# Kernel tuning notes

Measured on AMD Instinct MI355X. Metric: run time of the kernel, lower is better.

Reference implementation:

```python
import jax, jax.numpy as jnp
import numpy as np

LAMBDA = 0.01

def setup_inputs() -> dict:
    key = jax.random.key(0)
    x = jax.random.normal(key, (32, 16384, 64), dtype=jnp.float32)
    return {"x": x}

def reference(x):
    # x: (B, N, D)
    B, N, D = x.shape
    mean = jnp.mean(x, axis=1, keepdims=True)          # (B, 1, D)
    diffs = x - mean                                    # (B, N, D)
    # Fused covariance: sum of centered outer products == GEMM, no (B,N,D,D) blowup
    cov = jnp.einsum('bnd,bne->bde', diffs, diffs) / (N - 1)  # (B, D, D)
    cov = cov + LAMBDA * jnp.eye(D, dtype=x.dtype)
    # torch.unique on the flattened symmetric matrices == globally sorted set of the
    # B * D*(D+1)/2 distinct entries (duplicates only arise from symmetry, prob-1 for
    # continuous inputs). Extract upper triangle per batch, then global sort.
    iu, ju = jnp.triu_indices(D)
    tri = cov[:, iu, ju]                                # (B, d_out)
    d_out = D * (D + 1) // 2
    return jnp.sort(tri.reshape(-1)).reshape(B, d_out)
```

## Files before the change

### kernel.cpp

```cpp
#include <hip/hip_runtime.h>
#include <hip/hip_bf16.h>
#include <stdint.h>


#define BATCHES 32
#define NSAMP   16384
#define DIM     64
#define LAMBDA  0.01f
#define NTRI    2080
#define NOUT    (BATCHES * NTRI)

#define CHUNKS_PER_BATCH 32
#define SAMP_PER_BLOCK   (NSAMP / CHUNKS_PER_BATCH)
#define SAMP_PER_WAVE    (SAMP_PER_BLOCK / 4)
#define PARTIAL_STRIDE   2624

#define KEY_SHIFT 14
#define NBUCKET   (1 << 18)
#define SMALL_MAX 64u
#define SORT_CAP  8192

typedef __attribute__((ext_vector_type(4))) float f32x4;
typedef __attribute__((ext_vector_type(8))) short s16x8;

__device__ __forceinline__ uint32_t sort_key(float v) {
    uint32_t u = __builtin_bit_cast(uint32_t, v);
    return u ^ (uint32_t)(((int32_t)u >> 31) | 0x80000000u);
}

__device__ __forceinline__ uint32_t cvt_pk_bf16(float lo, float hi) {
    __hip_bfloat162 bb = __float22bfloat162_rn(make_float2(lo, hi));
    uint32_t u;
    __builtin_memcpy(&u, &bb, 4);
    return u;
}

__constant__ const int c_tmi[10] = {0, 0, 0, 0, 1, 1, 1, 2, 2, 3};
__constant__ const int c_tni[10] = {0, 1, 2, 3, 1, 2, 3, 2, 3, 3};

struct CovLds {
    float red[2][64][41];
    float msum_red[4][64];
};

template <typename EpilogueFn>
__device__ __forceinline__ void cov_body(const float* __restrict__ x, CovLds& L,
                                         EpilogueFn epi) {
    const int tid  = threadIdx.x;
    const int wave = tid >> 6;
    const int lane = tid & 63;
    const int b     = blockIdx.x / CHUNKS_PER_BATCH;
    const int chunk = blockIdx.x % CHUNKS_PER_BATCH;
    const int n_start = chunk * SAMP_PER_BLOCK + wave * SAMP_PER_WAVE;

    const int l15  = lane & 15;
    const int quad = lane >> 4;

    const float* xw = x + ((size_t)b * NSAMP + n_start) * DIM
                        + quad * 8 * DIM + l15;

    f32x4 acc[10];
#pragma unroll
    for (int t = 0; t < 10; ++t) acc[t] = (f32x4){0.f, 0.f, 0.f, 0.f};
    float sum_t[4] = {0.f, 0.f, 0.f, 0.f};

    float va[8][4], vb[8][4];

    auto loadit = [&](float (&v)[8][4], int kc) {
        const float* xs = xw + kc * 32 * DIM;
#pragma unroll
        for (int j = 0; j < 8; ++j)
#pragma unroll
            for (int t = 0; t < 4; ++t)
                v[j][t] = xs[j * DIM + t * 16];
    };

    auto compute = [&](float (&v)[8][4]) {
#pragma unroll
        for (int j = 0; j < 8; ++j)
#pragma unroll
            for (int t = 0; t < 4; ++t) sum_t[t] += v[j][t];

        s16x8 frag[4];
#pragma unroll
        for (int t = 0; t < 4; ++t) {
            uint32_t pk0 = cvt_pk_bf16(v[0][t], v[1][t]);
            uint32_t pk1 = cvt_pk_bf16(v[2][t], v[3][t]);
            uint32_t pk2 = cvt_pk_bf16(v[4][t], v[5][t]);
            uint32_t pk3 = cvt_pk_bf16(v[6][t], v[7][t]);
            frag[t] = __builtin_bit_cast(s16x8, make_uint4(pk0, pk1, pk2, pk3));
        }

        acc[0] = __builtin_amdgcn_mfma_f32_16x16x32_bf16(frag[0], frag[0], acc[0], 0, 0, 0);
        acc[1] = __builtin_amdgcn_mfma_f32_16x16x32_bf16(frag[0], frag[1], acc[1], 0, 0, 0);
        acc[2] = __builtin_amdgcn_mfma_f32_16x16x32_bf16(frag[0], frag[2], acc[2], 0, 0, 0);
        acc[3] = __builtin_amdgcn_mfma_f32_16x16x32_bf16(frag[0], frag[3], acc[3], 0, 0, 0);
        acc[4] = __builtin_amdgcn_mfma_f32_16x16x32_bf16(frag[1], frag[1], acc[4], 0, 0, 0);
        acc[5] = __builtin_amdgcn_mfma_f32_16x16x32_bf16(frag[1], frag[2], acc[5], 0, 0, 0);
        acc[6] = __builtin_amdgcn_mfma_f32_16x16x32_bf16(frag[1], frag[3], acc[6], 0, 0, 0);
        acc[7] = __builtin_amdgcn_mfma_f32_16x16x32_bf16(frag[2], frag[2], acc[7], 0, 0, 0);
        acc[8] = __builtin_amdgcn_mfma_f32_16x16x32_bf16(frag[2], frag[3], acc[8], 0, 0, 0);
        acc[9] = __builtin_amdgcn_mfma_f32_16x16x32_bf16(frag[3], frag[3], acc[9], 0, 0, 0);
    };

    loadit(va, 0);
    loadit(vb, 1);
    compute(va);
    loadit(va, 2);
    compute(vb);
    loadit(vb, 3);
    compute(va);
    compute(vb);

#pragma unroll
    for (int t = 0; t < 4; ++t) {
        sum_t[t] += __shfl_xor(sum_t[t], 16, 64);
        sum_t[t] += __shfl_xor(sum_t[t], 32, 64);
    }
    if (lane < 16) {
#pragma unroll
        for (int t = 0; t < 4; ++t) L.msum_red[wave][t * 16 + lane] = sum_t[t];
    }

    __syncthreads();
    if (wave == 1 || wave == 3) {
        int slot = wave >> 1;
#pragma unroll
        for (int t = 0; t < 10; ++t)
#pragma unroll
            for (int r = 0; r < 4; ++r) L.red[slot][lane][t * 4 + r] = acc[t][r];
    }
    __syncthreads();
    if (wave == 0 || wave == 2) {
        int slot = wave >> 1;
#pragma unroll
        for (int t = 0; t < 10; ++t)
#pragma unroll
            for (int r = 0; r < 4; ++r) acc[t][r] += L.red[slot][lane][t * 4 + r];
    }
    __syncthreads();
    if (wave == 2) {
#pragma unroll
        for (int t = 0; t < 10; ++t)
#pragma unroll
            for (int r = 0; r < 4; ++r) L.red[0][lane][t * 4 + r] = acc[t][r];
    }
    __syncthreads();
    if (wave == 0) {
#pragma unroll
        for (int t = 0; t < 10; ++t)
#pragma unroll
            for (int r = 0; r < 4; ++r) acc[t][r] += L.red[0][lane][t * 4 + r];
        float msum_tot = L.msum_red[0][lane] + L.msum_red[1][lane] +
                         L.msum_red[2][lane] + L.msum_red[3][lane];
        epi(b, lane, quad, l15, acc, msum_tot);
    }
}

__global__ __launch_bounds__(256, 3) void cov_kernel_p(const float* __restrict__ x,
                                                       float* __restrict__ partials,
                                                       uint32_t* __restrict__ hist,
                                                       uint32_t* __restrict__ counts) {
    hist[blockIdx.x * 256 + threadIdx.x] = 0u;
    if (blockIdx.x == 0 && threadIdx.x < 16) counts[threadIdx.x] = 0u;

    __shared__ CovLds L;
    float* Pb = partials + (size_t)blockIdx.x * PARTIAL_STRIDE;
    cov_body(x, L, [&](int b, int lane, int quad, int l15, f32x4* acc, float msum) {
#pragma unroll
        for (int t = 0; t < 10; ++t)
#pragma unroll
            for (int r = 0; r < 4; ++r)
                Pb[t * 256 + r * 64 + lane] = acc[t][r];
        Pb[2560 + lane] = msum;
    });
}

__global__ __launch_bounds__(256, 3) void cov_kernel_a(const float* __restrict__ x,
                                                       float* __restrict__ S,
                                                       float* __restrict__ Msum) {
    __shared__ CovLds L;
    cov_body(x, L, [&](int b, int lane, int quad, int l15, f32x4* acc, float msum) {
        float* Sb = S + b * DIM * DIM;
#pragma unroll
        for (int t = 0; t < 10; ++t) {
            int d0 = c_tmi[t] * 16 + quad * 4;
            int e  = c_tni[t] * 16 + l15;
#pragma unroll
            for (int r = 0; r < 4; ++r)
                atomicAdd(&Sb[(d0 + r) * DIM + e], acc[t][r]);
        }
        atomicAdd(&Msum[b * DIM + lane], msum);
    });
}

__global__ __launch_bounds__(256) void reduce_kernel(const float* __restrict__ partials,
                                                     float* __restrict__ tri,
                                                     uint32_t* __restrict__ hist) {
    const int b = blockIdx.x / 10, k = blockIdx.x % 10;
    const int tid = threadIdx.x;
    __shared__ float msum[DIM];
    const float* P0 = partials + (size_t)b * CHUNKS_PER_BATCH * PARTIAL_STRIDE;

    if (tid < DIM) {
        float ms = 0.f;
#pragma unroll
        for (int c = 0; c < CHUNKS_PER_BATCH; ++c)
            ms += P0[c * PARTIAL_STRIDE + 2560 + tid];
        msum[tid] = ms;
    }

    float a = 0.f;
#pragma unroll
    for (int c = 0; c < CHUNKS_PER_BATCH; ++c)
        a += P0[c * PARTIAL_STRIDE + k * 256 + tid];
    __syncthreads();

    const int r = tid >> 6, lane = tid & 63, quad = lane >> 4, l15 = lane & 15;
    const int row = c_tmi[k] * 16 + quad * 4 + r;
    const int col = c_tni[k] * 16 + l15;
    if (row <= col) {
        float v = (a - msum[row] * msum[col] * (1.0f / NSAMP)) * (1.0f / (NSAMP - 1));
        if (row == col) v += LAMBDA;
        int p = row * 64 - (row * (row + 1)) / 2 + col;
        tri[b * NTRI + p] = v;
        atomicAdd(&hist[sort_key(v) >> KEY_SHIFT], 1u);
    }
}

__global__ void finalize_kernel(const float* __restrict__ S,
                                const float* __restrict__ Msum,
                                float* __restrict__ tri,
                                uint32_t* __restrict__ hist) {
    int t = blockIdx.x * blockDim.x + threadIdx.x;
    int b = t >> 12, de = t & 4095, d = de >> 6, e = de & 63;
    if (d > e) return;
    float ssum = S[b * 4096 + d * 64 + e];
    float md = Msum[b * 64 + d], me = Msum[b * 64 + e];
    float v = (ssum - md * me * (1.0f / NSAMP)) * (1.0f / (NSAMP - 1));
    if (d == e) v += LAMBDA;
    int p = d * 64 - (d * (d + 1)) / 2 + e;
    tri[b * NTRI + p] = v;
    atomicAdd(&hist[sort_key(v) >> KEY_SHIFT], 1u);
}

__global__ __launch_bounds__(256) void scanA_kernel(const uint32_t* __restrict__ hist,
                                                    uint32_t* __restrict__ blocksums) {
    __shared__ uint32_t s[256];
    int tid = threadIdx.x;
    s[tid] = hist[blockIdx.x * 256 + tid];
    __syncthreads();
    for (int off = 128; off > 0; off >>= 1) {
        if (tid < off) s[tid] += s[tid + off];
        __syncthreads();
    }
    if (tid == 0) blocksums[blockIdx.x] = s[0];
}

__global__ __launch_bounds__(256) void scanB_kernel(const uint32_t* __restrict__ hist,
                                                    const uint32_t* __restrict__ blocksums,
                                                    uint32_t* __restrict__ offsets,
                                                    uint2* __restrict__ wl_small,
                                                    uint2* __restrict__ wl_large,
                                                    uint32_t* __restrict__ counts) {
    __shared__ uint32_t bs[256];
    __shared__ uint32_t sc[256];
    __shared__ uint32_t base_sh;
    int tid = threadIdx.x, bid = blockIdx.x;

    uint32_t b4[4]; uint32_t s4 = 0;
#pragma unroll
    for (int i = 0; i < 4; ++i) { b4[i] = blocksums[4 * tid + i]; s4 += b4[i]; }
    bs[tid] = s4;
    __syncthreads();
    for (int off = 1; off < 256; off <<= 1) {
        uint32_t a = (tid >= off) ? bs[tid - off] : 0u;
        __syncthreads();
        bs[tid] += a;
        __syncthreads();
    }
    if (tid == (bid >> 2)) {
        uint32_t base = (tid > 0) ? bs[tid - 1] : 0u;
        for (int i = 0; i < (bid & 3); ++i) base += b4[i];
        base_sh = base;
    }

    uint32_t v = hist[bid * 256 + tid];
    sc[tid] = v;
    __syncthreads();
    for (int off = 1; off < 256; off <<= 1) {
        uint32_t a = (tid >= off) ? sc[tid - off] : 0u;
        __syncthreads();
        sc[tid] += a;
        __syncthreads();
    }
    uint32_t excl = base_sh + sc[tid] - v;
    offsets[bid * 256 + tid] = excl;
    if (v >= 2u) {
        if (v <= SMALL_MAX) {
            uint32_t w = atomicAdd(&counts[0], 1u);
            wl_small[w] = make_uint2(excl, v);
        } else {
            uint32_t w = atomicAdd(&counts[1], 1u);
            wl_large[w] = make_uint2(excl, v);
        }
    }
}

__global__ void scatter_kernel(const float* __restrict__ tri,
                               uint32_t* __restrict__ offsets,
                               float* __restrict__ out) {
    int i = blockIdx.x * blockDim.x + threadIdx.x;
    if (i >= NOUT) return;
    float v = tri[i];
    uint32_t pos = atomicAdd(&offsets[sort_key(v) >> KEY_SHIFT], 1u);
    out[pos] = v;
}

__global__ __launch_bounds__(256) void runsort_kernel(float* __restrict__ out,
                                                      const uint2* __restrict__ wl_small,
                                                      const uint2* __restrict__ wl_large,
                                                      const uint32_t* __restrict__ counts) {
    __shared__ float buf[SORT_CAP];

    uint32_t nl = counts[1];
    for (uint32_t w = blockIdx.x; w < nl; w += gridDim.x) {
        uint2 ent = wl_large[w];
        uint32_t start = ent.x, cnt = ent.y;
        if (cnt > SORT_CAP) continue;
        uint32_t m = 1;
        while (m < cnt) m <<= 1;
        for (uint32_t i = threadIdx.x; i < m; i += blockDim.x)
            buf[i] = (i < cnt) ? out[start + i] : __builtin_inff();
        __syncthreads();
        for (uint32_t k = 2; k <= m; k <<= 1) {
            for (uint32_t j = k >> 1; j > 0; j >>= 1) {
                for (uint32_t i = threadIdx.x; i < m; i += blockDim.x) {
                    uint32_t ixj = i ^ j;
                    if (ixj > i) {
                        float a = buf[i], c = buf[ixj];
                        bool up = ((i & k) == 0u);
                        if ((a > c) == up) { buf[i] = c; buf[ixj] = a; }
                    }
                }
                __syncthreads();
            }
        }
        for (uint32_t i = threadIdx.x; i < cnt; i += blockDim.x)
            out[start + i] = buf[i];
        __syncthreads();
    }

    uint32_t ns = counts[0];
    int wave = threadIdx.x >> 6, lane = threadIdx.x & 63;
    for (uint32_t r = blockIdx.x * 4 + wave; r < ns; r += gridDim.x * 4) {
        uint2 e = wl_small[r];
        uint32_t start = e.x, cnt = e.y;
        float v = (lane < (int)cnt) ? out[start + lane] : __builtin_inff();
#pragma unroll
        for (uint32_t k = 2; k <= 64; k <<= 1)
            for (uint32_t j = k >> 1; j > 0; j >>= 1) {
                float p = __shfl_xor(v, (int)j, 64);
                bool keepmin = (((lane & k) == 0u) == ((lane & j) == 0u));
                v = keepmin ? fminf(v, p) : fmaxf(v, p);
            }
        if (lane < (int)cnt) out[start + lane] = v;
    }
}

static void launch_tail(uint32_t* hist, uint32_t* blocksums, uint32_t* offsets,
                        float* tri, uint2* wl_small, uint2* wl_large,
                        uint32_t* counts, float* out, hipStream_t stream) {
    scanA_kernel<<<NBUCKET / 256, 256, 0, stream>>>(hist, blocksums);
    scanB_kernel<<<NBUCKET / 256, 256, 0, stream>>>(hist, blocksums, offsets,
                                                    wl_small, wl_large, counts);
    scatter_kernel<<<(NOUT + 255) / 256, 256, 0, stream>>>(tri, offsets, out);
    runsort_kernel<<<1024, 256, 0, stream>>>(out, wl_small, wl_large, counts);
}

extern "C" void kernel_launch(void* const* d_in, const int* in_sizes, int n_in,
                              void* d_out, int out_size, void* d_ws, size_t ws_size,
                              hipStream_t stream) {
    const float* x = (const float*)d_in[0];
    float* out = (float*)d_out;
    char* ws = (char*)d_ws;

    const size_t NEED_P = 2666560 + (size_t)1024 * PARTIAL_STRIDE * 4;

    if (ws_size >= NEED_P) {
        uint32_t* hist      = (uint32_t*)(ws);
        uint32_t* counts    = (uint32_t*)(ws + 1048576);
        uint32_t* offsets   = (uint32_t*)(ws + 1048640);
        uint32_t* blocksums = (uint32_t*)(ws + 2097216);
        float*    tri       = (float*)(ws + 2101312);
        uint2*    wl_small  = (uint2*)(ws + 2367552);
        uint2*    wl_large  = (uint2*)(ws + 2633792);
        float*    partials  = (float*)(ws + 2666560);

        cov_kernel_p<<<BATCHES * CHUNKS_PER_BATCH, 256, 0, stream>>>(x, partials, hist, counts);
        reduce_kernel<<<BATCHES * 10, 256, 0, stream>>>(partials, tri, hist);
        launch_tail(hist, blocksums, offsets, tri, wl_small, wl_large, counts, out, stream);
    } else {
        float*    S         = (float*)(ws);
        float*    Msum      = (float*)(ws + 524288);
        uint32_t* hist      = (uint32_t*)(ws + 532480);
        uint32_t* counts    = (uint32_t*)(ws + 1581056);
        uint32_t* offsets   = (uint32_t*)(ws + 1581120);
        uint32_t* blocksums = (uint32_t*)(ws + 2629696);
        float*    tri       = (float*)(ws + 2633792);
        uint2*    wl_small  = (uint2*)(ws + 2900032);
        uint2*    wl_large  = (uint2*)(ws + 3166272);

        (void)hipMemsetAsync(d_ws, 0, 1581120, stream);
        cov_kernel_a<<<BATCHES * CHUNKS_PER_BATCH, 256, 0, stream>>>(x, S, Msum);
        finalize_kernel<<<(BATCHES * 4096) / 256, 256, 0, stream>>>(S, Msum, tri, hist);
        launch_tail(hist, blocksums, offsets, tri, wl_small, wl_large, counts, out, stream);
    }
}
```

Baseline: 302.2 us.

## Fuse reduce, scan, scatter and run-sort into one cooperative kernel with grid syncs

Replaces the five separate tail launches (reduce, scanA, scanB, scatter, runsort) with a single cooperative kernel of 512 persistent blocks that loops over work units and separates the phases with grid-wide syncs. The goal is to remove per-launch overhead and the idle gaps between the small dependent kernels. In exchange, each phase now runs on a fixed grid with grid.sync barriers and a union of LDS buffers, which can lower per-phase parallelism (e.g. scanA/scanB had 1024 blocks). It also depends on cooperative launch succeeding, and the launch's return value is ignored.

```diff
diff --git a/kernel.cpp b/kernel.cpp
--- a/kernel.cpp
+++ b/kernel.cpp
@@ -1,6 +1,9 @@
 #include <hip/hip_runtime.h>
 #include <hip/hip_bf16.h>
+#include <hip/hip_cooperative_groups.h>
 #include <stdint.h>
+
+namespace cg = cooperative_groups;
 
 
 #define BATCHES 32
@@ -19,6 +22,8 @@
 #define NBUCKET   (1 << 18)
 #define SMALL_MAX 64u
 #define SORT_CAP  8192
+
+#define TAIL_BLOCKS 512
 
 typedef __attribute__((ext_vector_type(4))) float f32x4;
 typedef __attribute__((ext_vector_type(8))) short s16x8;
@@ -194,12 +199,12 @@
     });
 }
 
-__global__ __launch_bounds__(256) void reduce_kernel(const float* __restrict__ partials,
-                                                     float* __restrict__ tri,
-                                                     uint32_t* __restrict__ hist) {
-    const int b = blockIdx.x / 10, k = blockIdx.x % 10;
-    const int tid = threadIdx.x;
-    __shared__ float msum[DIM];
+
+__device__ __forceinline__ void reduce_unit(const float* __restrict__ partials,
+                                            float* __restrict__ tri,
+                                            uint32_t* __restrict__ hist,
+                                            float* msum_sh, int unit, int tid) {
+    const int b = unit / 10, k = unit % 10;
     const float* P0 = partials + (size_t)b * CHUNKS_PER_BATCH * PARTIAL_STRIDE;
 
     if (tid < DIM) {
@@ -207,7 +212,7 @@
 #pragma unroll
         for (int c = 0; c < CHUNKS_PER_BATCH; ++c)
             ms += P0[c * PARTIAL_STRIDE + 2560 + tid];
-        msum[tid] = ms;
+        msum_sh[tid] = ms;
     }
 
     float a = 0.f;
@@ -220,54 +225,36 @@
     const int row = c_tmi[k] * 16 + quad * 4 + r;
     const int col = c_tni[k] * 16 + l15;
     if (row <= col) {
-        float v = (a - msum[row] * msum[col] * (1.0f / NSAMP)) * (1.0f / (NSAMP - 1));
+        float v = (a - msum_sh[row] * msum_sh[col] * (1.0f / NSAMP)) * (1.0f / (NSAMP - 1));
         if (row == col) v += LAMBDA;
         int p = row * 64 - (row * (row + 1)) / 2 + col;
         tri[b * NTRI + p] = v;
         atomicAdd(&hist[sort_key(v) >> KEY_SHIFT], 1u);
     }
-}
-
-__global__ void finalize_kernel(const float* __restrict__ S,
-                                const float* __restrict__ Msum,
-                                float* __restrict__ tri,
-                                uint32_t* __restrict__ hist) {
-    int t = blockIdx.x * blockDim.x + threadIdx.x;
-    int b = t >> 12, de = t & 4095, d = de >> 6, e = de & 63;
-    if (d > e) return;
-    float ssum = S[b * 4096 + d * 64 + e];
-    float md = Msum[b * 64 + d], me = Msum[b * 64 + e];
-    float v = (ssum - md * me * (1.0f / NSAMP)) * (1.0f / (NSAMP - 1));
-    if (d == e) v += LAMBDA;
-    int p = d * 64 - (d * (d + 1)) / 2 + e;
-    tri[b * NTRI + p] = v;
-    atomicAdd(&hist[sort_key(v) >> KEY_SHIFT], 1u);
-}
-
-__global__ __launch_bounds__(256) void scanA_kernel(const uint32_t* __restrict__ hist,
-                                                    uint32_t* __restrict__ blocksums) {
-    __shared__ uint32_t s[256];
-    int tid = threadIdx.x;
-    s[tid] = hist[blockIdx.x * 256 + tid];
+    __syncthreads();
+}
+
+__device__ __forceinline__ void scanA_unit(const uint32_t* __restrict__ hist,
+                                           uint32_t* __restrict__ blocksums,
+                                           uint32_t* s, int u, int tid) {
+    s[tid] = hist[u * 256 + tid];
     __syncthreads();
     for (int off = 128; off > 0; off >>= 1) {
         if (tid < off) s[tid] += s[tid + off];
         __syncthreads();
     }
-    if (tid == 0) blocksums[blockIdx.x] = s[0];
-}
-
-__global__ __launch_bounds__(256) void scanB_kernel(const uint32_t* __restrict__ hist,
-                                                    const uint32_t* __restrict__ blocksums,
-                                                    uint32_t* __restrict__ offsets,
-                                                    uint2* __restrict__ wl_small,
-                                                    uint2* __restrict__ wl_large,
-                                                    uint32_t* __restrict__ counts) {
-    __shared__ uint32_t bs[256];
-    __shared__ uint32_t sc[256];
-    __shared__ uint32_t base_sh;
-    int tid = threadIdx.x, bid = blockIdx.x;
-
+    if (tid == 0) blocksums[u] = s[0];
+    __syncthreads();
+}
+
+__device__ __forceinline__ void scanB_unit(const uint32_t* __restrict__ hist,
+                                           const uint32_t* __restrict__ blocksums,
+                                           uint32_t* __restrict__ offsets,
+                                           uint2* __restrict__ wl_small,
+                                           uint2* __restrict__ wl_large,
+                                           uint32_t* __restrict__ counts,
+                                           uint32_t* bs, uint32_t* sc,
+                                           uint32_t* base_sh, int u, int tid) {
     uint32_t b4[4]; uint32_t s4 = 0;
 #pragma unroll
     for (int i = 0; i < 4; ++i) { b4[i] = blocksums[4 * tid + i]; s4 += b4[i]; }
@@ -279,13 +266,13 @@
         bs[tid] += a;
         __syncthreads();
     }
-    if (tid == (bid >> 2)) {
+    if (tid == (u >> 2)) {
         uint32_t base = (tid > 0) ? bs[tid - 1] : 0u;
-        for (int i = 0; i < (bid & 3); ++i) base += b4[i];
-        base_sh = base;
-    }
-
-    uint32_t v = hist[bid * 256 + tid];
+        for (int i = 0; i < (u & 3); ++i) base += b4[i];
+        *base_sh = base;
+    }
+
+    uint32_t v = hist[u * 256 + tid];
     sc[tid] = v;
     __syncthreads();
     for (int off = 1; off < 256; off <<= 1) {
@@ -294,8 +281,8 @@
         sc[tid] += a;
         __syncthreads();
     }
-    uint32_t excl = base_sh + sc[tid] - v;
-    offsets[bid * 256 + tid] = excl;
+    uint32_t excl = *base_sh + sc[tid] - v;
+    offsets[u * 256 + tid] = excl;
     if (v >= 2u) {
         if (v <= SMALL_MAX) {
             uint32_t w = atomicAdd(&counts[0], 1u);
@@ -305,24 +292,14 @@
             wl_large[w] = make_uint2(excl, v);
         }
     }
-}
-
-__global__ void scatter_kernel(const float* __restrict__ tri,
-                               uint32_t* __restrict__ offsets,
-                               float* __restrict__ out) {
-    int i = blockIdx.x * blockDim.x + threadIdx.x;
-    if (i >= NOUT) return;
-    float v = tri[i];
-    uint32_t pos = atomicAdd(&offsets[sort_key(v) >> KEY_SHIFT], 1u);
-    out[pos] = v;
-}
-
-__global__ __launch_bounds__(256) void runsort_kernel(float* __restrict__ out,
-                                                      const uint2* __restrict__ wl_small,
-                                                      const uint2* __restrict__ wl_large,
-                                                      const uint32_t* __restrict__ counts) {
-    __shared__ float buf[SORT_CAP];
-
+    __syncthreads();
+}
+
+__device__ __forceinline__ void runsort_body(float* __restrict__ out,
+                                             const uint2* __restrict__ wl_small,
+                                             const uint2* __restrict__ wl_large,
+                                             const uint32_t* __restrict__ counts,
+                                             float* buf) {
     uint32_t nl = counts[1];
     for (uint32_t w = blockIdx.x; w < nl; w += gridDim.x) {
         uint2 ent = wl_large[w];
@@ -368,6 +345,99 @@
     }
 }
 
+union TailLds {
+    float    red_msum[DIM];
+    uint32_t scanA_s[256];
+    struct { uint32_t bs[256]; uint32_t sc[256]; uint32_t base; } sb;
+    float    buf[SORT_CAP];
+};
+
+__global__ __launch_bounds__(256, 2) void tail_kernel(
+        const float* __restrict__ partials, float* __restrict__ tri,
+        uint32_t* __restrict__ hist, uint32_t* __restrict__ blocksums,
+        uint32_t* __restrict__ offsets, uint2* __restrict__ wl_small,
+        uint2* __restrict__ wl_large, uint32_t* __restrict__ counts,
+        float* __restrict__ out) {
+    cg::grid_group grid = cg::this_grid();
+    __shared__ TailLds L;
+    const int tid = threadIdx.x;
+
+    for (int u = blockIdx.x; u < BATCHES * 10; u += gridDim.x)
+        reduce_unit(partials, tri, hist, L.red_msum, u, tid);
+    grid.sync();
+
+    for (int u = blockIdx.x; u < NBUCKET / 256; u += gridDim.x)
+        scanA_unit(hist, blocksums, L.scanA_s, u, tid);
+    grid.sync();
+
+    for (int u = blockIdx.x; u < NBUCKET / 256; u += gridDim.x)
+        scanB_unit(hist, blocksums, offsets, wl_small, wl_large, counts,
+                   L.sb.bs, L.sb.sc, &L.sb.base, u, tid);
+    grid.sync();
+
+    for (int i = blockIdx.x * 256 + tid; i < NOUT; i += gridDim.x * 256) {
+        float v = tri[i];
+        uint32_t pos = atomicAdd(&offsets[sort_key(v) >> KEY_SHIFT], 1u);
+        out[pos] = v;
+    }
+    grid.sync();
+
+    runsort_body(out, wl_small, wl_large, counts, L.buf);
+}
+
+__global__ void finalize_kernel(const float* __restrict__ S,
+                                const float* __restrict__ Msum,
+                                float* __restrict__ tri,
+                                uint32_t* __restrict__ hist) {
+    int t = blockIdx.x * blockDim.x + threadIdx.x;
+    int b = t >> 12, de = t & 4095, d = de >> 6, e = de & 63;
+    if (d > e) return;
+    float ssum = S[b * 4096 + d * 64 + e];
+    float md = Msum[b * 64 + d], me = Msum[b * 64 + e];
+    float v = (ssum - md * me * (1.0f / NSAMP)) * (1.0f / (NSAMP - 1));
+    if (d == e) v += LAMBDA;
+    int p = d * 64 - (d * (d + 1)) / 2 + e;
+    tri[b * NTRI + p] = v;
+    atomicAdd(&hist[sort_key(v) >> KEY_SHIFT], 1u);
+}
+
+__global__ __launch_bounds__(256) void scanA_kernel(const uint32_t* __restrict__ hist,
+                                                    uint32_t* __restrict__ blocksums) {
+    __shared__ uint32_t s[256];
+    scanA_unit(hist, blocksums, s, blockIdx.x, threadIdx.x);
+}
+
+__global__ __launch_bounds__(256) void scanB_kernel(const uint32_t* __restrict__ hist,
+                                                    const uint32_t* __restrict__ blocksums,
+                                                    uint32_t* __restrict__ offsets,
+                                                    uint2* __restrict__ wl_small,
+                                                    uint2* __restrict__ wl_large,
+                                                    uint32_t* __restrict__ counts) {
+    __shared__ uint32_t bs[256];
+    __shared__ uint32_t sc[256];
+    __shared__ uint32_t base_sh;
+    scanB_unit(hist, blocksums, offsets, wl_small, wl_large, counts,
+               bs, sc, &base_sh, blockIdx.x, threadIdx.x);
+}
+
+__global__ void scatter_kernel(const float* __restrict__ tri,
+                               uint32_t* __restrict__ offsets,
+                               float* __restrict__ out) {
+    int i = blockIdx.x * blockDim.x + threadIdx.x;
+    if (i >= NOUT) return;
+    float v = tri[i];
+    uint32_t pos = atomicAdd(&offsets[sort_key(v) >> KEY_SHIFT], 1u);
+    out[pos] = v;
+}
+
+__global__ __launch_bounds__(256) void runsort_kernel(float* __restrict__ out,
+                                                      const uint2* __restrict__ wl_small,
+                                                      const uint2* __restrict__ wl_large,
+                                                      const uint32_t* __restrict__ counts) {
+    __shared__ float buf[SORT_CAP];
+    runsort_body(out, wl_small, wl_large, counts, buf);
+}
+
 static void launch_tail(uint32_t* hist, uint32_t* blocksums, uint32_t* offsets,
                         float* tri, uint2* wl_small, uint2* wl_large,
                         uint32_t* counts, float* out, hipStream_t stream) {
@@ -398,8 +468,11 @@
         float*    partials  = (float*)(ws + 2666560);
 
         cov_kernel_p<<<BATCHES * CHUNKS_PER_BATCH, 256, 0, stream>>>(x, partials, hist, counts);
-        reduce_kernel<<<BATCHES * 10, 256, 0, stream>>>(partials, tri, hist);
-        launch_tail(hist, blocksums, offsets, tri, wl_small, wl_large, counts, out, stream);
+
+        void* args[9] = {&partials, &tri, &hist, &blocksums, &offsets,
+                         &wl_small, &wl_large, &counts, &out};
+        (void)hipLaunchCooperativeKernel(reinterpret_cast<void*>(tail_kernel),
+                                         dim3(TAIL_BLOCKS), dim3(256), args, 0, stream);
     } else {
         float*    S         = (float*)(ws);
         float*    Msum      = (float*)(ws + 524288);
```

New measurement: 464.3 us. +53.6%, slower.

## Replace two-pass histogram scan with single-pass decoupled look-back scan

Applied to the files above, without the earlier changes.

Merges the scanA/scanB pair into one scan kernel that uses decoupled look-back. Each block publishes its aggregate or inclusive prefix through a flag-tagged word in scan_state, and one wave per block spins over its predecessors. The scan_state words are zeroed in the covariance kernel. This removes one kernel launch and the blocksums round trip. The cost is spin-waiting, which depends on blocks being scheduled roughly in index order.

```diff
diff --git a/kernel.cpp b/kernel.cpp
--- a/kernel.cpp
+++ b/kernel.cpp
@@ -17,6 +17,7 @@
 
 #define KEY_SHIFT 14
 #define NBUCKET   (1 << 18)
+#define SCAN_BLOCKS (NBUCKET / 256)
 #define SMALL_MAX 64u
 #define SORT_CAP  8192
 
@@ -160,8 +161,10 @@
 __global__ __launch_bounds__(256, 3) void cov_kernel_p(const float* __restrict__ x,
                                                        float* __restrict__ partials,
                                                        uint32_t* __restrict__ hist,
-                                                       uint32_t* __restrict__ counts) {
+                                                       uint32_t* __restrict__ counts,
+                                                       uint32_t* __restrict__ scan_state) {
     hist[blockIdx.x * 256 + threadIdx.x] = 0u;
+    if (threadIdx.x == 0) scan_state[blockIdx.x] = 0u;
     if (blockIdx.x == 0 && threadIdx.x < 16) counts[threadIdx.x] = 0u;
 
     __shared__ CovLds L;
@@ -244,6 +247,92 @@
     atomicAdd(&hist[sort_key(v) >> KEY_SHIFT], 1u);
 }
 
+__global__ __launch_bounds__(256) void scan_kernel(const uint32_t* __restrict__ hist,
+                                                   uint32_t* __restrict__ offsets,
+                                                   uint32_t* __restrict__ scan_state,
+                                                   uint2* __restrict__ wl_small,
+                                                   uint2* __restrict__ wl_large,
+                                                   uint32_t* __restrict__ counts) {
+    __shared__ uint32_t sc[256];
+    __shared__ uint32_t base_sh;
+    const int u = blockIdx.x, tid = threadIdx.x;
+
+    uint32_t v = hist[u * 256 + tid];
+    sc[tid] = v;
+    __syncthreads();
+    for (int off = 1; off < 256; off <<= 1) {
+        uint32_t a = (tid >= off) ? sc[tid - off] : 0u;
+        __syncthreads();
+        sc[tid] += a;
+        __syncthreads();
+    }
+    const uint32_t total = sc[255];
+
+    if (tid == 0) {
+        uint32_t pack = total | ((u == 0) ? 0x80000000u : 0x40000000u);
+        __hip_atomic_store(&scan_state[u], pack, __ATOMIC_RELEASE,
+                           __HIP_MEMORY_SCOPE_AGENT);
+        if (u == 0) base_sh = 0u;
+    }
+
+    if (u > 0 && tid < 64) {
+        const int lane = tid;
+        uint32_t excl = 0;
+        int j = u - 1;
+        for (;;) {
+            int idx = j - lane;
+            uint32_t s;
+            if (idx >= 0)
+                s = __hip_atomic_load(&scan_state[idx], __ATOMIC_ACQUIRE,
+                                      __HIP_MEMORY_SCOPE_AGENT);
+            else
+                s = 0x80000000u;
+            uint32_t st = s >> 30;
+            uint64_t pref = __ballot(st >= 2u);
+            uint64_t valid = __ballot(st >= 1u);
+            if (pref == 0ull) {
+                if (valid == ~0ull) {
+                    uint32_t val = s & 0x3FFFFFFFu;
+#pragma unroll
+                    for (int o = 1; o < 64; o <<= 1) val += __shfl_xor(val, o, 64);
+                    excl += val;
+                    j -= 64;
+                    continue;
+                }
+                __builtin_amdgcn_s_sleep(2);
+                continue;
+            }
+            int L = __ffsll((unsigned long long)pref) - 1;
+            uint64_t need = (L == 0) ? 0ull : ((1ull << L) - 1ull);
+            if ((valid & need) != need) { __builtin_amdgcn_s_sleep(2); continue; }
+            uint32_t val = (lane <= L) ? (s & 0x3FFFFFFFu) : 0u;
+#pragma unroll
+            for (int o = 1; o < 64; o <<= 1) val += __shfl_xor(val, o, 64);
+            excl += val;
+            break;
+        }
+        if (lane == 0) {
+            __hip_atomic_store(&scan_state[u],
+                               ((excl + total) & 0x3FFFFFFFu) | 0x80000000u,
+                               __ATOMIC_RELEASE, __HIP_MEMORY_SCOPE_AGENT);
+            base_sh = excl;
+        }
+    }
+    __syncthreads();
+
+    uint32_t excl = base_sh + sc[tid] - v;
+    offsets[u * 256 + tid] = excl;
+    if (v >= 2u) {
+        if (v <= SMALL_MAX) {
+            uint32_t w = atomicAdd(&counts[0], 1u);
+            wl_small[w] = make_uint2(excl, v);
+        } else {
+            uint32_t w = atomicAdd(&counts[1], 1u);
+            wl_large[w] = make_uint2(excl, v);
+        }
+    }
+}
+
 __global__ __launch_bounds__(256) void scanA_kernel(const uint32_t* __restrict__ hist,
                                                     uint32_t* __restrict__ blocksums) {
     __shared__ uint32_t s[256];
@@ -368,16 +457,6 @@
     }
 }
 
-static void launch_tail(uint32_t* hist, uint32_t* blocksums, uint32_t* offsets,
-                        float* tri, uint2* wl_small, uint2* wl_large,
-                        uint32_t* counts, float* out, hipStream_t stream) {
-    scanA_kernel<<<NBUCKET / 256, 256, 0, stream>>>(hist, blocksums);
-    scanB_kernel<<<NBUCKET / 256, 256, 0, stream>>>(hist, blocksums, offsets,
-                                                    wl_small, wl_large, counts);
-    scatter_kernel<<<(NOUT + 255) / 256, 256, 0, stream>>>(tri, offsets, out);
-    runsort_kernel<<<1024, 256, 0, stream>>>(out, wl_small, wl_large, counts);
-}
-
 extern "C" void kernel_launch(void* const* d_in, const int* in_sizes, int n_in,
                               void* d_out, int out_size, void* d_ws, size_t ws_size,
                               hipStream_t stream) {
@@ -388,18 +467,22 @@
     const size_t NEED_P = 2666560 + (size_t)1024 * PARTIAL_STRIDE * 4;
 
     if (ws_size >= NEED_P) {
-        uint32_t* hist      = (uint32_t*)(ws);
-        uint32_t* counts    = (uint32_t*)(ws + 1048576);
-        uint32_t* offsets   = (uint32_t*)(ws + 1048640);
-        uint32_t* blocksums = (uint32_t*)(ws + 2097216);
-        float*    tri       = (float*)(ws + 2101312);
-        uint2*    wl_small  = (uint2*)(ws + 2367552);
-        uint2*    wl_large  = (uint2*)(ws + 2633792);
-        float*    partials  = (float*)(ws + 2666560);
-
-        cov_kernel_p<<<BATCHES * CHUNKS_PER_BATCH, 256, 0, stream>>>(x, partials, hist, counts);
+        uint32_t* hist       = (uint32_t*)(ws);
+        uint32_t* counts     = (uint32_t*)(ws + 1048576);
+        uint32_t* offsets    = (uint32_t*)(ws + 1048640);
+        uint32_t* scan_state = (uint32_t*)(ws + 2097216);
+        float*    tri        = (float*)(ws + 2101312);
+        uint2*    wl_small   = (uint2*)(ws + 2367552);
+        uint2*    wl_large   = (uint2*)(ws + 2633792);
+        float*    partials   = (float*)(ws + 2666560);
+
+        cov_kernel_p<<<BATCHES * CHUNKS_PER_BATCH, 256, 0, stream>>>(x, partials, hist,
+                                                                     counts, scan_state);
         reduce_kernel<<<BATCHES * 10, 256, 0, stream>>>(partials, tri, hist);
-        launch_tail(hist, blocksums, offsets, tri, wl_small, wl_large, counts, out, stream);
+        scan_kernel<<<SCAN_BLOCKS, 256, 0, stream>>>(hist, offsets, scan_state,
+                                                     wl_small, wl_large, counts);
+        scatter_kernel<<<(NOUT + 255) / 256, 256, 0, stream>>>(tri, offsets, out);
+        runsort_kernel<<<1024, 256, 0, stream>>>(out, wl_small, wl_large, counts);
     } else {
         float*    S         = (float*)(ws);
         float*    Msum      = (float*)(ws + 524288);
@@ -414,6 +497,10 @@
         (void)hipMemsetAsync(d_ws, 0, 1581120, stream);
         cov_kernel_a<<<BATCHES * CHUNKS_PER_BATCH, 256, 0, stream>>>(x, S, Msum);
         finalize_kernel<<<(BATCHES * 4096) / 256, 256, 0, stream>>>(S, Msum, tri, hist);
-        launch_tail(hist, blocksums, offsets, tri, wl_small, wl_large, counts, out, stream);
-    }
-}
+        scanA_kernel<<<NBUCKET / 256, 256, 0, stream>>>(hist, blocksums);
+        scanB_kernel<<<NBUCKET / 256, 256, 0, stream>>>(hist, blocksums, offsets,
+                                                        wl_small, wl_large, counts);
+        scatter_kernel<<<(NOUT + 255) / 256, 256, 0, stream>>>(tri, offsets, out);
+        runsort_kernel<<<1024, 256, 0, stream>>>(out, wl_small, wl_large, counts);
+    }
+}
```

Result: slower. 334.0 us (+10.5%).
